# Performance work log

Hardware: AMD Instinct MI355X
Metric: run time of the kernel (lower is better)

## Reference

```python
import jax, jax.numpy as jnp
import numpy as np

NUM_CLASSES = 1000
FEAT_DIM = 256
MOMENTUM = 0.999
WARMUP_STEPS = 200


def setup_inputs() -> dict:
    key = jax.random.key(0)
    k1, k2, k3, k4, k5 = jax.random.split(key, 5)
    N, B, K = 200000, 64, 100
    features = jax.random.normal(k1, (N, FEAT_DIM), jnp.float32)
    labels = jax.random.randint(k2, (N,), 0, NUM_CLASSES)
    labels_per_image = jax.random.randint(k3, (B, K), 0, NUM_CLASSES)
    prototypes = jax.random.normal(k4, (NUM_CLASSES, FEAT_DIM), jnp.float32)
    init_mask = jax.random.randint(k5, (NUM_CLASSES,), 0, 2).astype(jnp.int32)
    cooccurrence = jnp.zeros((NUM_CLASSES, NUM_CLASSES), jnp.float32)
    return dict(features=features, labels=labels, labels_per_image=labels_per_image,
                prototypes=prototypes, init_mask=init_mask, cooccurrence=cooccurrence,
                step=5000)


def reference(features, labels, labels_per_image, prototypes, init_mask, cooccurrence, step):
    C = prototypes.shape[0]
    progress = min(1.0, float(step) / max(1, WARMUP_STEPS * 10))
    m = 0.99 + (MOMENTUM - 0.99) * progress

    # F.normalize(features, dim=-1) with eps=1e-12
    fn = features / jnp.clip(jnp.linalg.norm(features, axis=-1, keepdims=True), 1e-12)

    # per-class scatter-mean (replaces Python loop over labels.unique())
    counts = jax.ops.segment_sum(jnp.ones(labels.shape, jnp.float32), labels, num_segments=C)  # [C]
    sums = jax.ops.segment_sum(fn, labels, num_segments=C)                                      # [C, D]
    mean = sums / jnp.maximum(counts, 1.0)[:, None]

    present = (counts > 0)[:, None]          # class appears in this batch
    inited = (init_mask > 0)[:, None]        # prototype already initialized
    ema = m * prototypes + (1.0 - m) * mean
    new_protos = jnp.where(present & inited, ema, jnp.where(present & ~inited, mean, prototypes))
    new_init = ((init_mask > 0) | (counts > 0)).astype(jnp.int32)

    # co-occurrence: presence matrix P[B,C]; pair (ci,cj) gets +1 each direction per image
    B, K = labels_per_image.shape
    rows = jnp.repeat(jnp.arange(B), K)
    P = jnp.zeros((B, C), jnp.float32).at[rows, labels_per_image.reshape(-1)].set(1.0)
    cooc_add = (P.T @ P) * (1.0 - jnp.eye(C, dtype=jnp.float32))
    new_cooc = cooccurrence + cooc_add

    return new_protos, new_init, new_cooc
```

## Files before the change

kernel.cpp:

```cpp
#include <hip/hip_runtime.h>
#include <hip/hip_bf16.h>

#define NC 1000
#define FD 256
#define KPI 100
#define CAP 1024

__global__ void k_scatter(const int* __restrict__ labels, int n,
                          const int* __restrict__ lpi, int bk,
                          int* __restrict__ cursor,
                          unsigned long long* __restrict__ M,
                          int* __restrict__ rowidx) {
    int i = blockIdx.x * blockDim.x + threadIdx.x;
    if (i < n) {
        int lab = labels[i];
        int pos = atomicAdd(&cursor[lab], 1);
        if (pos < CAP) rowidx[lab * CAP + pos] = i;
    }
    if (i < bk) atomicOr(&M[lpi[i]], 1ull << (i / KPI));
}

__global__ __launch_bounds__(256) void k_proto(
    const float* __restrict__ feat, const int* __restrict__ rowidx,
    const int* __restrict__ cursor,
    const float* __restrict__ protos, const int* __restrict__ init_mask,
    const int* __restrict__ step,
    const unsigned long long* __restrict__ M,
    const float* __restrict__ cooc_in,
    float* __restrict__ out_protos, float* __restrict__ out_init,
    float* __restrict__ out_cooc) {
    int c = blockIdx.x;
    int tid = threadIdx.x;
    int lane = tid & 63;
    int w = tid >> 6;
    int cnt = cursor[c];
    if (cnt > CAP) cnt = CAP;
    int start = c * CAP;
    int end = start + cnt;

    const float4* f4 = (const float4*)feat;
    float ax = 0.f, ay = 0.f, az = 0.f, aw = 0.f;

    for (int base = start + 4 * w; base < end; base += 16) {
        int r[4];
        float4 v[4];
        float s[4];
        #pragma unroll
        for (int k = 0; k < 4; k++) {
            int idx = (base + k < end) ? (base + k) : (end - 1);
            r[k] = rowidx[idx];
        }
        #pragma unroll
        for (int k = 0; k < 4; k++) v[k] = f4[(size_t)r[k] * 64 + lane];
        #pragma unroll
        for (int k = 0; k < 4; k++)
            s[k] = v[k].x * v[k].x + v[k].y * v[k].y + v[k].z * v[k].z + v[k].w * v[k].w;
        #pragma unroll
        for (int o = 32; o; o >>= 1) {
            #pragma unroll
            for (int k = 0; k < 4; k++) s[k] += __shfl_xor(s[k], o);
        }
        #pragma unroll
        for (int k = 0; k < 4; k++) {
            float sc = (base + k < end) ? (1.0f / fmaxf(sqrtf(s[k]), 1e-12f)) : 0.0f;
            ax += v[k].x * sc;
            ay += v[k].y * sc;
            az += v[k].z * sc;
            aw += v[k].w * sc;
        }
    }

    __shared__ float4 sh4[256];
    sh4[w * 64 + lane] = make_float4(ax, ay, az, aw);
    __syncthreads();

    const float* shf = (const float*)sh4;
    int d = tid;
    float t = shf[d] + shf[256 + d] + shf[512 + d] + shf[768 + d];
    float mean = t / fmaxf((float)cnt, 1.0f);

    float p = protos[c * FD + d];
    bool present = cnt > 0;
    bool inited = init_mask[c] > 0;
    float prog = fminf(1.0f, (float)step[0] / 2000.0f);
    float m = 0.99f + (0.999f - 0.99f) * prog;
    float ema = m * p + (1.0f - m) * mean;
    float outv = present ? (inited ? ema : mean) : p;
    out_protos[c * FD + d] = outv;
    if (tid == 0) out_init[c] = (inited || present) ? 1.0f : 0.0f;

    unsigned long long mi = M[c];
    for (int j = tid; j < NC; j += 256) {
        float add = (c == j) ? 0.0f : (float)__popcll(mi & M[j]);
        out_cooc[c * NC + j] = cooc_in[c * NC + j] + add;
    }
}

extern "C" void kernel_launch(void* const* d_in, const int* in_sizes, int n_in,
                              void* d_out, int out_size, void* d_ws, size_t ws_size,
                              hipStream_t stream) {
    const float* feat      = (const float*)d_in[0];
    const int*   labels    = (const int*)d_in[1];
    const int*   lpi       = (const int*)d_in[2];
    const float* protos    = (const float*)d_in[3];
    const int*   init_mask = (const int*)d_in[4];
    const float* cooc      = (const float*)d_in[5];
    const int*   step      = (const int*)d_in[6];

    int n  = in_sizes[1];
    int bk = in_sizes[2];

    float* out_protos = (float*)d_out;
    float* out_init   = out_protos + (size_t)NC * FD;
    float* out_cooc   = out_init + NC;

    char* ws = (char*)d_ws;
    int* cursor           = (int*)(ws);
    unsigned long long* M = (unsigned long long*)(ws + 4096);
    int* rowidx           = (int*)(ws + 12288);

    hipMemsetAsync(d_ws, 0, 12288, stream);

    int big = n > bk ? n : bk;
    k_scatter<<<(big + 255) / 256, 256, 0, stream>>>(labels, n, lpi, bk, cursor, M, rowidx);
    k_proto<<<NC, 256, 0, stream>>>(feat, rowidx, cursor, protos, init_mask, step,
                                    M, cooc, out_protos, out_init, out_cooc);
}
```

Measured before the change: 347.0 us.

## Fuse memset, scatter and prototype kernels into one cooperative kernel with grid syncs

Replaces the workspace memset plus two kernel launches with a single cooperative kernel of NC blocks. The kernel zeroes the cursors and masks, scatters labels with a grid-stride loop, and computes prototypes and co-occurrence, with grid.sync between phases. This removes launch and memset overhead, but the label scatter now runs on only 1000 blocks and the grid-wide barriers add cost. A cooperative launch also requires all 1000 blocks to be co-resident on the device.

New measurement: 501.5 us. 1.45x slower.

```diff
diff --git a/kernel.cpp b/kernel.cpp
--- a/kernel.cpp
+++ b/kernel.cpp
@@ -1,36 +1,48 @@
 #include <hip/hip_runtime.h>
 #include <hip/hip_bf16.h>
+#include <hip/hip_cooperative_groups.h>
+
+namespace cg = cooperative_groups;
 
 #define NC 1000
 #define FD 256
 #define KPI 100
 #define CAP 1024
 
-__global__ void k_scatter(const int* __restrict__ labels, int n,
-                          const int* __restrict__ lpi, int bk,
-                          int* __restrict__ cursor,
-                          unsigned long long* __restrict__ M,
-                          int* __restrict__ rowidx) {
-    int i = blockIdx.x * blockDim.x + threadIdx.x;
-    if (i < n) {
+__global__ __launch_bounds__(256) void k_fused(
+    const float* __restrict__ feat,
+    const int* __restrict__ labels, int n,
+    const int* __restrict__ lpi, int bk,
+    const float* __restrict__ protos,
+    const int* __restrict__ init_mask,
+    const int* __restrict__ step,
+    const float* __restrict__ cooc_in,
+    int* __restrict__ cursor,
+    unsigned long long* __restrict__ M,
+    int* __restrict__ rowidx,
+    float* __restrict__ out_protos,
+    float* __restrict__ out_init,
+    float* __restrict__ out_cooc) {
+    cg::grid_group grid = cg::this_grid();
+    int tid = threadIdx.x;
+    int gid = blockIdx.x * 256 + tid;
+
+    if (blockIdx.x == 0) {
+        for (int i = tid; i < NC; i += 256) cursor[i] = 0;
+    } else if (blockIdx.x == 1) {
+        for (int i = tid; i < NC; i += 256) M[i] = 0ull;
+    }
+    grid.sync();
+
+    for (int i = gid; i < n; i += gridDim.x * 256) {
         int lab = labels[i];
         int pos = atomicAdd(&cursor[lab], 1);
         if (pos < CAP) rowidx[lab * CAP + pos] = i;
     }
-    if (i < bk) atomicOr(&M[lpi[i]], 1ull << (i / KPI));
-}
+    if (gid < bk) atomicOr(&M[lpi[gid]], 1ull << (gid / KPI));
+    grid.sync();
 
-__global__ __launch_bounds__(256) void k_proto(
-    const float* __restrict__ feat, const int* __restrict__ rowidx,
-    const int* __restrict__ cursor,
-    const float* __restrict__ protos, const int* __restrict__ init_mask,
-    const int* __restrict__ step,
-    const unsigned long long* __restrict__ M,
-    const float* __restrict__ cooc_in,
-    float* __restrict__ out_protos, float* __restrict__ out_init,
-    float* __restrict__ out_cooc) {
     int c = blockIdx.x;
-    int tid = threadIdx.x;
     int lane = tid & 63;
     int w = tid >> 6;
     int cnt = cursor[c];
@@ -119,10 +131,12 @@
     unsigned long long* M = (unsigned long long*)(ws + 4096);
     int* rowidx           = (int*)(ws + 12288);
 
-    hipMemsetAsync(d_ws, 0, 12288, stream);
-
-    int big = n > bk ? n : bk;
-    k_scatter<<<(big + 255) / 256, 256, 0, stream>>>(labels, n, lpi, bk, cursor, M, rowidx);
-    k_proto<<<NC, 256, 0, stream>>>(feat, rowidx, cursor, protos, init_mask, step,
-                                    M, cooc, out_protos, out_init, out_cooc);
+    void* args[] = {
+        (void*)&feat, (void*)&labels, (void*)&n, (void*)&lpi, (void*)&bk,
+        (void*)&protos, (void*)&init_mask, (void*)&step, (void*)&cooc,
+        (void*)&cursor, (void*)&M, (void*)&rowidx,
+        (void*)&out_protos, (void*)&out_init, (void*)&out_cooc
+    };
+    hipLaunchCooperativeKernel(reinterpret_cast<void*>(k_fused),
+                               dim3(NC), dim3(256), args, 0, stream);
 }
```

## Split per-class prototype reduction across four blocks with last-block finalize

Applied to the files above, without the earlier changes.

Each class is now handled by four blocks. Each block gathers and normalizes a strided quarter of that class's feature rows, writes its partial sums to a workspace buffer, and increments an atomic counter. The last block to finish sums the partials and writes the prototype update. The co-occurrence row is also split across the four blocks, and launch bounds now request higher occupancy. This aims to raise parallelism and hide memory latency in the gather, which was limited to 1000 blocks. The cost is the extra partial-sum traffic, the fences and the atomic handshake.

New measurement: 1.190 ms. 243% more time.

```diff
diff --git a/kernel.cpp b/kernel.cpp
--- a/kernel.cpp
+++ b/kernel.cpp
@@ -5,6 +5,7 @@
 #define FD 256
 #define KPI 100
 #define CAP 1024
+#define SPLIT 4
 
 __global__ void k_scatter(const int* __restrict__ labels, int n,
                           const int* __restrict__ lpi, int bk,
@@ -20,16 +21,19 @@
     if (i < bk) atomicOr(&M[lpi[i]], 1ull << (i / KPI));
 }
 
-__global__ __launch_bounds__(256) void k_proto(
+__global__ __launch_bounds__(256, 8) void k_proto(
     const float* __restrict__ feat, const int* __restrict__ rowidx,
     const int* __restrict__ cursor,
     const float* __restrict__ protos, const int* __restrict__ init_mask,
     const int* __restrict__ step,
     const unsigned long long* __restrict__ M,
     const float* __restrict__ cooc_in,
+    float* __restrict__ partial, int* __restrict__ done,
     float* __restrict__ out_protos, float* __restrict__ out_init,
     float* __restrict__ out_cooc) {
-    int c = blockIdx.x;
+    int blk = blockIdx.x;
+    int c = blk / SPLIT;
+    int h = blk % SPLIT;
     int tid = threadIdx.x;
     int lane = tid & 63;
     int w = tid >> 6;
@@ -41,7 +45,7 @@
     const float4* f4 = (const float4*)feat;
     float ax = 0.f, ay = 0.f, az = 0.f, aw = 0.f;
 
-    for (int base = start + 4 * w; base < end; base += 16) {
+    for (int base = start + 4 * (h * 4 + w); base < end; base += 4 * 16) {
         int r[4];
         float4 v[4];
         float s[4];
@@ -70,14 +74,33 @@
         }
     }
 
+    unsigned long long mi = M[c];
+    if (tid < NC / SPLIT) {
+        int j = h * (NC / SPLIT) + tid;
+        float add = (c == j) ? 0.0f : (float)__popcll(mi & M[j]);
+        out_cooc[c * NC + j] = cooc_in[c * NC + j] + add;
+    }
+
     __shared__ float4 sh4[256];
     sh4[w * 64 + lane] = make_float4(ax, ay, az, aw);
     __syncthreads();
-
     const float* shf = (const float*)sh4;
     int d = tid;
     float t = shf[d] + shf[256 + d] + shf[512 + d] + shf[768 + d];
-    float mean = t / fmaxf((float)cnt, 1.0f);
+
+    partial[(size_t)blk * FD + d] = t;
+    __threadfence();
+    __syncthreads();
+    __shared__ int last;
+    if (tid == 0) last = (atomicAdd(&done[c], 1) == SPLIT - 1) ? 1 : 0;
+    __syncthreads();
+    if (!last) return;
+    __threadfence();
+
+    float sum = 0.f;
+    #pragma unroll
+    for (int q = 0; q < SPLIT; q++) sum += partial[(size_t)(c * SPLIT + q) * FD + d];
+    float mean = sum / fmaxf((float)cnt, 1.0f);
 
     float p = protos[c * FD + d];
     bool present = cnt > 0;
@@ -88,12 +111,6 @@
     float outv = present ? (inited ? ema : mean) : p;
     out_protos[c * FD + d] = outv;
     if (tid == 0) out_init[c] = (inited || present) ? 1.0f : 0.0f;
-
-    unsigned long long mi = M[c];
-    for (int j = tid; j < NC; j += 256) {
-        float add = (c == j) ? 0.0f : (float)__popcll(mi & M[j]);
-        out_cooc[c * NC + j] = cooc_in[c * NC + j] + add;
-    }
 }
 
 extern "C" void kernel_launch(void* const* d_in, const int* in_sizes, int n_in,
@@ -117,12 +134,15 @@
     char* ws = (char*)d_ws;
     int* cursor           = (int*)(ws);
     unsigned long long* M = (unsigned long long*)(ws + 4096);
-    int* rowidx           = (int*)(ws + 12288);
+    int* done             = (int*)(ws + 12288);
+    int* rowidx           = (int*)(ws + 16384);
+    float* partial        = (float*)(ws + 16384 + (size_t)NC * CAP * 4);
 
-    hipMemsetAsync(d_ws, 0, 12288, stream);
+    hipMemsetAsync(d_ws, 0, 16384, stream);
 
     int big = n > bk ? n : bk;
     k_scatter<<<(big + 255) / 256, 256, 0, stream>>>(labels, n, lpi, bk, cursor, M, rowidx);
-    k_proto<<<NC, 256, 0, stream>>>(feat, rowidx, cursor, protos, init_mask, step,
-                                    M, cooc, out_protos, out_init, out_cooc);
+    k_proto<<<NC * SPLIT, 256, 0, stream>>>(feat, rowidx, cursor, protos, init_mask, step,
+                                            M, cooc, partial, done,
+                                            out_protos, out_init, out_cooc);
 }
```
